# Kernel optimization log

Hardware: AMD Instinct MI355X
Metric: run time of the kernel (lower is better)

Reference implementation:

```python
import jax, jax.numpy as jnp
import numpy as np
from jax import lax

GAP_PENALTY = 0.0
TEMPERATURE = 1.0
B, A, L, D, K = 64, 26, 384, 512, 18


def setup_inputs() -> dict:
    key = jax.random.key(0)
    k1, k2, k3, k4 = jax.random.split(key, 4)
    matrices = jax.random.normal(k1, (B, A, L), dtype=jnp.float32)
    # ragged lengths: (len_i, len_0) per pair, in [L//2, L]
    shapes = jax.random.randint(k2, (B, 2), L // 2, L + 1, dtype=jnp.int32)
    s = 1.0 / np.sqrt(A * K)  # torch Conv1d default init scale
    conv_w = jax.random.uniform(k3, (D, A, K), minval=-s, maxval=s, dtype=jnp.float32)
    conv_b = jax.random.uniform(k4, (D,), minval=-s, maxval=s, dtype=jnp.float32)
    return {"matrices": matrices, "shapes": shapes, "conv_w": conv_w, "conv_b": conv_b}


def _smoothmax3(a, b, c, t):
    # t * log(exp(a/t) + exp(b/t) + exp(c/t)), numerically stable
    m = jnp.maximum(jnp.maximum(a, b), c)
    return m + t * jnp.log(jnp.exp((a - m) / t) + jnp.exp((b - m) / t) + jnp.exp((c - m) / t))


def _nw_matrix(sim, t, g):
    # sim: (L, L). Returns smoothed NW value matrix V: (L+1, L+1).
    # V[i,j] = sim[i-1,j-1] + smoothmax(V[i-1,j-1], V[i-1,j]-g, V[i,j-1]-g)
    n = sim.shape[0]
    row0 = -g * jnp.arange(n + 1, dtype=sim.dtype)  # free/affine leading gaps on top row

    def row_step(prev_row, inp):
        s_row, i = inp  # s_row: (L,)
        v_left0 = -g * i  # V[i, 0]

        def col_step(left, xs):
            s, diag, up = xs
            v = s + _smoothmax3(diag, up - g, left - g, t)
            return v, v

        _, rest = lax.scan(col_step, v_left0, (s_row, prev_row[:-1], prev_row[1:]))
        new_row = jnp.concatenate([v_left0[None], rest])
        return new_row, new_row

    _, rows = lax.scan(row_step, row0, (sim, jnp.arange(1, n + 1, dtype=sim.dtype)))
    return jnp.concatenate([row0[None], rows], axis=0)


def needleman_wunsch(sim, shapes, gap_penalty, temperature):
    # sim: (B, L, L) similarity vs sequence 0; shapes: (B, 2) int lengths.
    # Soft alignment posterior = grad of smoothed terminal score wrt similarity.
    li = jnp.clip(shapes[:, 0], 0, sim.shape[1])
    lj = jnp.clip(shapes[:, 1], 0, sim.shape[2])

    def total_score(s):
        V = jax.vmap(lambda m: _nw_matrix(m, temperature, gap_penalty))(s)  # (B, L+1, L+1)
        b = jnp.arange(s.shape[0])
        return jnp.sum(V[b, li, lj])

    return jax.grad(total_score)(sim)  # (B, L, L), expected match matrix


def reference(matrices, shapes, conv_w, conv_b):
    # Conv1d padding='same' with even kernel: torch pads (k-1)//2 left, k//2 right
    k = conv_w.shape[-1]
    pad = ((k - 1) // 2, k // 2)
    emb = lax.conv_general_dilated(
        matrices, conv_w, window_strides=(1,), padding=[pad],
        dimension_numbers=("NCH", "OIH", "NCH"),
    ) + conv_b[None, :, None]  # (B, D, L)
    e = jnp.transpose(emb, (0, 2, 1))  # (B, L, D)
    sim = jnp.einsum("bld,md->blm", e, e[0])  # (B, L_i, L_0): similarity vs sequence 0
    align = needleman_wunsch(sim, shapes, GAP_PENALTY, TEMPERATURE)  # (B, L, L)
    m = jnp.transpose(matrices, (0, 2, 1))  # (B, L, A)
    # consensus in sequence-0 coordinates, then project back to each sequence
    consensus = jnp.mean(jnp.einsum("nia,nij->nja", m, align), axis=0)  # (L, A)
    return jnp.einsum("ja,nij->nia", consensus, align)  # (B, L, A)
```

## Files before the change

kernel.cpp:

```cpp
#include <hip/hip_runtime.h>
#include <hip/hip_bf16.h>
#include <math.h>

#define B_  64
#define A_  26
#define L_  384
#define D_  512
#define K_  18
#define KC  480
#define LL  147456
#define SZD 245760

typedef __attribute__((ext_vector_type(8))) short bf16x8;
typedef __attribute__((ext_vector_type(4))) float f32x4;
typedef unsigned short ushort_t;
typedef unsigned int uint_t;

__device__ __forceinline__ void stD(float* sp, int z, int c, float v) {
    int dl = z / 6, dr = z - dl * 6;
    sp[(size_t)(dl + (c >> 2)) * 1536 + dr * 256 + dl * 4 + (c & 3)] = v;
}

__device__ __forceinline__ ushort_t f2bf(float v) {
    uint_t u = __float_as_uint(v);
    uint_t r = (u + 0x7FFFu + ((u >> 16) & 1u)) >> 16;
    return (ushort_t)r;
}

__global__ void wsplit_kernel(const float* __restrict__ w, ushort_t* __restrict__ wh,
                              ushort_t* __restrict__ wl) {
    int o = blockIdx.x * blockDim.x + threadIdx.x;
    if (o >= D_ * KC) return;
    int d = o / KC, r = o - d * KC;
    float v = (r < A_ * K_) ? w[(size_t)d * (A_ * K_) + r] : 0.0f;
    ushort_t h = f2bf(v);
    float hf = __uint_as_float(((uint_t)h) << 16);
    size_t oo = ((size_t)(r >> 5) * D_ + d) * 32 + (r & 31);
    wh[oo] = h;
    wl[oo] = f2bf(v - hf);
}

__global__ __launch_bounds__(256) void im2col_kernel(const float* __restrict__ x,
                                                     ushort_t* __restrict__ xh,
                                                     ushort_t* __restrict__ xl) {
    int b  = blockIdx.y;
    int lt = blockIdx.x;
    const float* xb = x + (size_t)b * A_ * L_;
    for (int idx = threadIdx.x; idx < 64 * KC; idx += 256) {
        int l = lt * 64 + idx / KC;
        int r = idx % KC;
        float v = 0.0f;
        if (r < A_ * K_) {
            int a = r / K_, kk = r - a * K_;
            int g = l + kk - 8;
            if (g >= 0 && g < L_) v = xb[(size_t)a * L_ + g];
        }
        ushort_t h = f2bf(v);
        float hf = __uint_as_float(((uint_t)h) << 16);
        size_t o = (((size_t)b * 15 + (r >> 5)) * L_ + l) * 32 + (r & 31);
        xh[o] = h;
        xl[o] = f2bf(v - hf);
    }
}

__global__ __launch_bounds__(256) void convmm_kernel(const ushort_t* __restrict__ xh,
                                                     const ushort_t* __restrict__ xl,
                                                     const ushort_t* __restrict__ wh,
                                                     const ushort_t* __restrict__ wl,
                                                     const float* __restrict__ bias,
                                                     ushort_t* __restrict__ ehi,
                                                     ushort_t* __restrict__ elo) {
    int b = blockIdx.z;
    int w = threadIdx.x >> 6;
    int lane = threadIdx.x & 63;
    int l0 = blockIdx.y * 64 + 32 * (w >> 1);
    int d0 = blockIdx.x * 64 + 32 * (w & 1);
    int r = lane & 15, g = lane >> 4;
    const ushort_t* pah = xh + (((size_t)b * 15) * L_ + l0 + r) * 32 + g * 8;
    const ushort_t* pal = xl + (((size_t)b * 15) * L_ + l0 + r) * 32 + g * 8;
    const ushort_t* pbh = wh + (size_t)(d0 + r) * 32 + g * 8;
    const ushort_t* pbl = wl + (size_t)(d0 + r) * 32 + g * 8;
    f32x4 acc00 = {0.f, 0.f, 0.f, 0.f}, acc01 = acc00, acc10 = acc00, acc11 = acc00;
#pragma unroll 3
    for (int ks = 0; ks < 15; ++ks) {
        size_t offA = (size_t)ks * L_ * 32;
        size_t offB = (size_t)ks * D_ * 32;
        bf16x8 Ah0 = *(const bf16x8*)(pah + offA);
        bf16x8 Ah1 = *(const bf16x8*)(pah + offA + 16 * 32);
        bf16x8 Al0 = *(const bf16x8*)(pal + offA);
        bf16x8 Al1 = *(const bf16x8*)(pal + offA + 16 * 32);
        bf16x8 Bh0 = *(const bf16x8*)(pbh + offB);
        bf16x8 Bh1 = *(const bf16x8*)(pbh + offB + 16 * 32);
        bf16x8 Bl0 = *(const bf16x8*)(pbl + offB);
        bf16x8 Bl1 = *(const bf16x8*)(pbl + offB + 16 * 32);
        acc00 = __builtin_amdgcn_mfma_f32_16x16x32_bf16(Ah0, Bh0, acc00, 0, 0, 0);
        acc00 = __builtin_amdgcn_mfma_f32_16x16x32_bf16(Ah0, Bl0, acc00, 0, 0, 0);
        acc00 = __builtin_amdgcn_mfma_f32_16x16x32_bf16(Al0, Bh0, acc00, 0, 0, 0);
        acc01 = __builtin_amdgcn_mfma_f32_16x16x32_bf16(Ah0, Bh1, acc01, 0, 0, 0);
        acc01 = __builtin_amdgcn_mfma_f32_16x16x32_bf16(Ah0, Bl1, acc01, 0, 0, 0);
        acc01 = __builtin_amdgcn_mfma_f32_16x16x32_bf16(Al0, Bh1, acc01, 0, 0, 0);
        acc10 = __builtin_amdgcn_mfma_f32_16x16x32_bf16(Ah1, Bh0, acc10, 0, 0, 0);
        acc10 = __builtin_amdgcn_mfma_f32_16x16x32_bf16(Ah1, Bl0, acc10, 0, 0, 0);
        acc10 = __builtin_amdgcn_mfma_f32_16x16x32_bf16(Al1, Bh0, acc10, 0, 0, 0);
        acc11 = __builtin_amdgcn_mfma_f32_16x16x32_bf16(Ah1, Bh1, acc11, 0, 0, 0);
        acc11 = __builtin_amdgcn_mfma_f32_16x16x32_bf16(Ah1, Bl1, acc11, 0, 0, 0);
        acc11 = __builtin_amdgcn_mfma_f32_16x16x32_bf16(Al1, Bh1, acc11, 0, 0, 0);
    }
#pragma unroll
    for (int v = 0; v < 4; ++v) {
        int lr0 = l0 + g * 4 + v, lr1 = lr0 + 16;
        int dc0 = d0 + r,         dc1 = dc0 + 16;
        float vals[4] = {acc00[v] + bias[dc0], acc01[v] + bias[dc1],
                         acc10[v] + bias[dc0], acc11[v] + bias[dc1]};
        int lrs[4] = {lr0, lr0, lr1, lr1};
        int dcs[4] = {dc0, dc1, dc0, dc1};
#pragma unroll
        for (int t = 0; t < 4; ++t) {
            ushort_t h = f2bf(vals[t]);
            float hf = __uint_as_float(((uint_t)h) << 16);
            size_t o = (((size_t)b * 16 + (dcs[t] >> 5)) * L_ + lrs[t]) * 32 + (dcs[t] & 31);
            ehi[o] = h;
            elo[o] = f2bf(vals[t] - hf);
        }
    }
}

__global__ __launch_bounds__(256) void sim_kernel(const ushort_t* __restrict__ ehi,
                                                  const ushort_t* __restrict__ elo,
                                                  float* __restrict__ simD) {
    int b = blockIdx.z;
    int w = threadIdx.x >> 6;
    int lane = threadIdx.x & 63;
    int l0 = blockIdx.y * 64 + 32 * (w >> 1);
    int m0 = blockIdx.x * 64 + 32 * (w & 1);
    int r = lane & 15, g = lane >> 4;
    const ushort_t* pah = ehi + (((size_t)b * 16) * L_ + l0 + r) * 32 + g * 8;
    const ushort_t* pal = elo + (((size_t)b * 16) * L_ + l0 + r) * 32 + g * 8;
    const ushort_t* pbh = ehi + ((size_t)(m0 + r)) * 32 + g * 8;
    const ushort_t* pbl = elo + ((size_t)(m0 + r)) * 32 + g * 8;
    f32x4 acc00 = {0.f, 0.f, 0.f, 0.f}, acc01 = acc00, acc10 = acc00, acc11 = acc00;
#pragma unroll 2
    for (int ks = 0; ks < 16; ++ks) {
        size_t off = (size_t)ks * L_ * 32;
        bf16x8 Ah0 = *(const bf16x8*)(pah + off);
        bf16x8 Ah1 = *(const bf16x8*)(pah + off + 16 * 32);
        bf16x8 Al0 = *(const bf16x8*)(pal + off);
        bf16x8 Al1 = *(const bf16x8*)(pal + off + 16 * 32);
        bf16x8 Bh0 = *(const bf16x8*)(pbh + off);
        bf16x8 Bh1 = *(const bf16x8*)(pbh + off + 16 * 32);
        bf16x8 Bl0 = *(const bf16x8*)(pbl + off);
        bf16x8 Bl1 = *(const bf16x8*)(pbl + off + 16 * 32);
        acc00 = __builtin_amdgcn_mfma_f32_16x16x32_bf16(Ah0, Bh0, acc00, 0, 0, 0);
        acc00 = __builtin_amdgcn_mfma_f32_16x16x32_bf16(Ah0, Bl0, acc00, 0, 0, 0);
        acc00 = __builtin_amdgcn_mfma_f32_16x16x32_bf16(Al0, Bh0, acc00, 0, 0, 0);
        acc01 = __builtin_amdgcn_mfma_f32_16x16x32_bf16(Ah0, Bh1, acc01, 0, 0, 0);
        acc01 = __builtin_amdgcn_mfma_f32_16x16x32_bf16(Ah0, Bl1, acc01, 0, 0, 0);
        acc01 = __builtin_amdgcn_mfma_f32_16x16x32_bf16(Al0, Bh1, acc01, 0, 0, 0);
        acc10 = __builtin_amdgcn_mfma_f32_16x16x32_bf16(Ah1, Bh0, acc10, 0, 0, 0);
        acc10 = __builtin_amdgcn_mfma_f32_16x16x32_bf16(Ah1, Bl0, acc10, 0, 0, 0);
        acc10 = __builtin_amdgcn_mfma_f32_16x16x32_bf16(Al1, Bh0, acc10, 0, 0, 0);
        acc11 = __builtin_amdgcn_mfma_f32_16x16x32_bf16(Ah1, Bh1, acc11, 0, 0, 0);
        acc11 = __builtin_amdgcn_mfma_f32_16x16x32_bf16(Ah1, Bl1, acc11, 0, 0, 0);
        acc11 = __builtin_amdgcn_mfma_f32_16x16x32_bf16(Al1, Bh1, acc11, 0, 0, 0);
    }
    float* sp = simD + (size_t)b * SZD;
#pragma unroll
    for (int v = 0; v < 4; ++v) {
        int ar0 = l0 + g * 4 + v, ar1 = ar0 + 16;
        int ac0 = m0 + r,         ac1 = ac0 + 16;
        stD(sp, ar0, ac0, acc00[v]);
        stD(sp, ar0, ac1, acc01[v]);
        stD(sp, ar1, ac0, acc10[v]);
        stD(sp, ar1, ac1, acc11[v]);
    }
}

__global__ __launch_bounds__(256, 1) void nw_fwd_kernel(const float* __restrict__ simD, float* __restrict__ VD) {
    int b = blockIdx.x;
    int tid = threadIdx.x;
    int w = tid >> 6, l = tid & 63;
    __shared__ float4 MA[4][64], MB4[4][64], MC[4][64];
    __shared__ int FL[4];
    const float4 Z4 = {0.f, 0.f, 0.f, 0.f};
    {
        int s = tid >> 6, ll = tid & 63;
        MA[s][ll] = Z4; MB4[s][ll] = Z4; MC[s][ll] = Z4;
    }
    if (tid < 4) FL[tid] = (tid == 3) ? -1 : -1000000;
    __syncthreads();
    volatile int* flg = FL;
    const float* pS = simD + (size_t)b * SZD + l * 4;
    float*       pV = VD   + (size_t)b * SZD + l * 4;
    float4 buf[6];
#pragma unroll
    for (int r = 0; r < 6; ++r) buf[r] = *(const float4*)(pS + w * 1536 + r * 256);
    int lm = (l == 0) ? 0 : (l - 1);
#pragma unroll 1
    for (int T = w; T < 159; T += 4) {
        int sp = (T - 1) & 3;
        while (flg[sp] != T - 1) {}
        asm volatile("" ::: "memory");
        float4 Ar = MA[sp][l];
        float4 Bs = MB4[sp][l];
        float4 Cs = MC[sp][l];
        float4 Bn = MB4[sp][lm];
        float4 Cn = MC[sp][lm];
        if (l == 0) { Bn = Z4; Cn = Z4; }
        float vleft[6] = {Ar.x, Ar.y, Ar.z, Ar.w, Bs.x, Bs.y};
        float d0 = Bn.z;
        float uin[4] = {Cn.x, Cn.y, Cn.z, Cn.w};
        float sc[6][4];
#pragma unroll
        for (int r = 0; r < 6; ++r) {
            sc[r][0] = buf[r].x; sc[r][1] = buf[r].y; sc[r][2] = buf[r].z; sc[r][3] = buf[r].w;
        }
        int ct = T - l;
        bool act = (ct >= 0 && ct <= 95);
        float nbc[4] = {0.f, 0.f, 0.f, 0.f}, nbp = 0.f;
        float vout[6][4];
        if (act) {
#pragma unroll
            for (int dd = 0; dd < 9; ++dd) {
#pragma unroll
                for (int r = 0; r < 6; ++r) {
                    const int q = dd - r;
                    if (q < 0 || q > 3) continue;
                    float dg = (r == 0) ? ((q == 0) ? d0 : uin[q - 1])
                                        : ((q == 0) ? vleft[r - 1] : vout[r - 1][q - 1]);
                    float up = (r == 0) ? uin[q] : vout[r - 1][q];
                    float lf = (q == 0) ? vleft[r] : vout[r][q - 1];
                    float mx = fmaxf(dg, fmaxf(up, lf));
                    vout[r][q] = sc[r][q] + mx +
                        __logf(__expf(dg - mx) + __expf(up - mx) + __expf(lf - mx));
                }
            }
            nbp = Cs.w;
#pragma unroll
            for (int q = 0; q < 4; ++q) nbc[q] = vout[5][q];
#pragma unroll
            for (int r = 0; r < 6; ++r) vleft[r] = vout[r][3];
        }
        float4 pa; pa.x = vleft[0]; pa.y = vleft[1]; pa.z = vleft[2]; pa.w = vleft[3];
        float4 pb; pb.x = vleft[4]; pb.y = vleft[5]; pb.z = nbp; pb.w = 0.f;
        float4 pc; pc.x = nbc[0]; pc.y = nbc[1]; pc.z = nbc[2]; pc.w = nbc[3];
        MA[w][l] = pa; MB4[w][l] = pb; MC[w][l] = pc;
        asm volatile("s_waitcnt lgkmcnt(0)" ::: "memory");
        if (l == 0) flg[w] = T;
        asm volatile("" ::: "memory");
        if (act) {
            float* pVd = pV + (size_t)T * 1536;
#pragma unroll
            for (int r = 0; r < 6; ++r) {
                float4 t;
                t.x = vout[r][0]; t.y = vout[r][1]; t.z = vout[r][2]; t.w = vout[r][3];
                *(float4*)(pVd + r * 256) = t;
            }
        }
        int dP = min(T + 4, 158);
#pragma unroll
        for (int r = 0; r < 6; ++r) buf[r] = *(const float4*)(pS + dP * 1536 + r * 256);
    }
}

__global__ __launch_bounds__(256, 1) void nw_bwd_kernel(const float* __restrict__ simD,
                                                        const float* __restrict__ VD,
                                                        const int* __restrict__ shapes,
                                                        float* __restrict__ ED) {
    int b = blockIdx.x;
    int tid = threadIdx.x;
    int w = tid >> 6, l = tid & 63;
    __shared__ float4 MA[4][64], MB4[4][64], MC[4][64], MD[4][64], MEx[4][64], MF[4][64];
    __shared__ int FL[4];
    const float4 Z4 = {0.f, 0.f, 0.f, 0.f};
    {
        int s = tid >> 6, ll = tid & 63;
        MA[s][ll] = Z4; MB4[s][ll] = Z4; MC[s][ll] = Z4;
        MD[s][ll] = Z4; MEx[s][ll] = Z4; MF[s][ll] = Z4;
    }
    if (tid < 4) FL[tid] = (tid == 3) ? -1 : -1000000;
    __syncthreads();
    volatile int* flg = FL;
    const float* pS = simD + (size_t)b * SZD + l * 4;
    const float* pV = VD   + (size_t)b * SZD + l * 4;
    float*       pE = ED   + (size_t)b * SZD + l * 4;
    int li = min(max(shapes[2 * b + 0], 0), L_);
    int lj = min(max(shapes[2 * b + 1], 0), L_);
    float4 bufV[6], bufS[6];
#pragma unroll
    for (int r = 0; r < 6; ++r) {
        bufV[r] = *(const float4*)(pV + (158 - w) * 1536 + r * 256);
        bufS[r] = *(const float4*)(pS + (158 - w) * 1536 + r * 256);
    }
    int lp = (l == 63) ? 63 : (l + 1);
#pragma unroll 1
    for (int T = w; T < 159; T += 4) {
        int sp = (T - 1) & 3;
        while (flg[sp] != T - 1) {}
        asm volatile("" ::: "memory");
        float4 Ar = MA[sp][l];
        float4 Br = MB4[sp][l];
        float4 Cr = MC[sp][l];
        float4 Dn = MD[sp][lp];
        float4 En = MEx[sp][lp];
        float4 Fn = MF[sp][lp];
        if (l == 63) { Dn = Z4; En = Z4; Fn = Z4; }
        float einit[6] = {Ar.x, Ar.y, Ar.z, Ar.w, Br.x, Br.y};
        float uinit[6] = {Br.z, Br.w, Cr.x, Cr.y, Cr.z, Cr.w};
        float enb_c[4] = {Dn.x, Dn.y, Dn.z, Dn.w};
        float unb_c[4] = {En.x, En.y, En.z, En.w};
        float enbtd_s = Fn.x, unbtd_s = Fn.y;
        float Vq[6][4], Sq[6][4];
#pragma unroll
        for (int r = 0; r < 6; ++r) {
            Vq[r][0] = bufV[r].x; Vq[r][1] = bufV[r].y; Vq[r][2] = bufV[r].z; Vq[r][3] = bufV[r].w;
            Sq[r][0] = bufS[r].x; Sq[r][1] = bufS[r].y; Sq[r][2] = bufS[r].z; Sq[r][3] = bufS[r].w;
        }
        int ct = 158 - T - l;
        bool act = (ct >= 0 && ct <= 95);
        float necar[4] = {0.f, 0.f, 0.f, 0.f}, nucar[4] = {0.f, 0.f, 0.f, 0.f};
        float eC[6], uC[6];
#pragma unroll
        for (int r = 0; r < 6; ++r) { eC[r] = einit[r]; uC[r] = uinit[r]; }
        float Eo[6][4];
        if (act) {
            float Uo[6][4];
#pragma unroll
            for (int r = 0; r < 6; ++r)
#pragma unroll
                for (int q = 0; q < 4; ++q)
                    Uo[r][q] = Vq[r][q] - Sq[r][q];
            float wtd[6][4], wtu[6][4], wtl[6][4];
#pragma unroll
            for (int r = 0; r < 6; ++r) {
                int i = 6 * l + r + 1;
                bool ilt = (i < L_);
#pragma unroll
                for (int q = 0; q < 4; ++q) {
                    int j = 4 * ct + q + 1;
                    bool jlt = (j < L_);
                    float ub_old = (r == 5) ? ((q == 3) ? unbtd_s : unb_c[q + 1])
                                            : ((q == 3) ? uinit[r + 1] : Uo[r + 1][q + 1]);
                    float ub_new = (r == 5) ? unb_c[q] : Uo[r + 1][q];
                    float uo_r   = (q == 3) ? uinit[r] : Uo[r][q + 1];
                    wtd[r][q] = (ilt && jlt) ? __expf(Vq[r][q] - ub_old) : 0.f;
                    wtu[r][q] = ilt ? __expf(Vq[r][q] - ub_new) : 0.f;
                    wtl[r][q] = jlt ? __expf(Vq[r][q] - uo_r) : 0.f;
                }
            }
#pragma unroll
            for (int dd = 0; dd < 9; ++dd) {
#pragma unroll
                for (int r = 5; r >= 0; --r) {
                    const int q = 8 - dd - r;
                    if (q < 0 || q > 3) continue;
                    int i = 6 * l + r + 1;
                    int j = 4 * ct + q + 1;
                    float eb_old = (r == 5) ? ((q == 3) ? enbtd_s : enb_c[q + 1])
                                            : ((q == 3) ? einit[r + 1] : Eo[r + 1][q + 1]);
                    float eb_new = (r == 5) ? enb_c[q] : Eo[r + 1][q];
                    float eo_r   = (q == 3) ? einit[r] : Eo[r][q + 1];
                    float en = (i == li && j == lj) ? 1.f : 0.f;
                    en += wtd[r][q] * eb_old + wtu[r][q] * eb_new + wtl[r][q] * eo_r;
                    Eo[r][q] = en;
                }
            }
#pragma unroll
            for (int r = 0; r < 6; ++r) { eC[r] = Eo[r][0]; uC[r] = Uo[r][0]; }
#pragma unroll
            for (int q = 0; q < 4; ++q) { necar[q] = Eo[0][q]; nucar[q] = Uo[0][q]; }
        }
        float4 pa; pa.x = eC[0]; pa.y = eC[1]; pa.z = eC[2]; pa.w = eC[3];
        float4 pb; pb.x = eC[4]; pb.y = eC[5]; pb.z = uC[0]; pb.w = uC[1];
        float4 pc; pc.x = uC[2]; pc.y = uC[3]; pc.z = uC[4]; pc.w = uC[5];
        float4 pd; pd.x = necar[0]; pd.y = necar[1]; pd.z = necar[2]; pd.w = necar[3];
        float4 pe; pe.x = nucar[0]; pe.y = nucar[1]; pe.z = nucar[2]; pe.w = nucar[3];
        float4 pf; pf.x = einit[0]; pf.y = uinit[0]; pf.z = 0.f; pf.w = 0.f;
        MA[w][l] = pa; MB4[w][l] = pb; MC[w][l] = pc;
        MD[w][l] = pd; MEx[w][l] = pe; MF[w][l] = pf;
        asm volatile("s_waitcnt lgkmcnt(0)" ::: "memory");
        if (l == 0) flg[w] = T;
        asm volatile("" ::: "memory");
        if (act) {
            float* pEd = pE + (size_t)(158 - T) * 1536;
#pragma unroll
            for (int r = 0; r < 6; ++r) {
                float4 t;
                t.x = Eo[r][0]; t.y = Eo[r][1]; t.z = Eo[r][2]; t.w = Eo[r][3];
                *(float4*)(pEd + r * 256) = t;
            }
        }
        int dP = max(158 - (T + 4), 0);
#pragma unroll
        for (int r = 0; r < 6; ++r) {
            bufV[r] = *(const float4*)(pV + dP * 1536 + r * 256);
            bufS[r] = *(const float4*)(pS + dP * 1536 + r * 256);
        }
    }
}

__global__ __launch_bounds__(256) void repack_kernel(const float* __restrict__ ED,
                                                     float* __restrict__ Enat) {
    int n  = blockIdx.y;
    int jt = blockIdx.x;
    int jl = threadIdx.x & 63;
    int gp = threadIdx.x >> 6;
    int j  = jt * 64 + jl;
    const float* eb = ED + (size_t)n * SZD + (j >> 2) * 1536 + (j & 3);
    float* ob = Enat + (size_t)n * LL + j;
#pragma unroll 4
    for (int i = gp * 96; i < gp * 96 + 96; ++i) {
        int dl = i / 6, dr = i - dl * 6;
        float v = eb[(size_t)dl * 1540 + dr * 256];
        ob[(size_t)i * L_] = v;
    }
}

__global__ __launch_bounds__(256) void consensus_kernel(const float* __restrict__ x,
                                                        const float* __restrict__ Enat,
                                                        float* __restrict__ cons) {
    int n  = blockIdx.y;
    int j0 = blockIdx.x * 64;
    __shared__ float ms[A_][L_];
    for (int idx = threadIdx.x; idx < A_ * L_; idx += 256)
        ((float*)ms)[idx] = x[(size_t)n * A_ * L_ + idx];
    __syncthreads();
    int jl = threadIdx.x & 63;
    int g  = threadIdx.x >> 6;
    int a0 = g * 7;
    int na = (a0 + 7 <= A_) ? 7 : (A_ - a0);
    int j  = j0 + jl;
    float acc[7] = {0.f, 0.f, 0.f, 0.f, 0.f, 0.f, 0.f};
    const float* aE = Enat + (size_t)n * LL + j;
    for (int i = 0; i < L_; ++i) {
        float al = aE[(size_t)i * L_];
#pragma unroll
        for (int t = 0; t < 7; ++t)
            if (t < na) acc[t] = fmaf(al, ms[a0 + t][i], acc[t]);
    }
    for (int t = 0; t < na; ++t)
        atomicAdd(&cons[(size_t)j * A_ + a0 + t], acc[t] * (1.0f / B_));
}

__global__ __launch_bounds__(256) void out_kernel(const float* __restrict__ Enat,
                                                  const float* __restrict__ cons,
                                                  float* __restrict__ out) {
    int n  = blockIdx.y;
    int i0 = blockIdx.x * 32;
    __shared__ float cs[L_][A_];
    __shared__ float as_[32][L_ + 1];
    for (int idx = threadIdx.x; idx < L_ * A_; idx += 256)
        ((float*)cs)[idx] = cons[idx];
    const float* aE = Enat + (size_t)n * LL;
    for (int idx = threadIdx.x; idx < 32 * L_; idx += 256) {
        int r = idx / L_, c = idx - r * L_;
        as_[r][c] = aE[(size_t)(i0 + r) * L_ + c];
    }
    __syncthreads();
    for (int o = threadIdx.x; o < 32 * A_; o += 256) {
        int il = o / A_, a = o % A_;
        float s = 0.f;
        for (int jj = 0; jj < L_; ++jj)
            s = fmaf(as_[il][jj], cs[jj][a], s);
        out[((size_t)n * L_ + i0 + il) * A_ + a] = s;
    }
}

extern "C" void kernel_launch(void* const* d_in, const int* in_sizes, int n_in,
                              void* d_out, int out_size, void* d_ws, size_t ws_size,
                              hipStream_t stream) {
    const float* matrices = (const float*)d_in[0];
    const int*   shapes   = (const int*)d_in[1];
    const float* conv_w   = (const float*)d_in[2];
    const float* conv_b   = (const float*)d_in[3];
    float* out = (float*)d_out;

    char* p = (char*)d_ws;
    float*    EDiag = (float*)p;
    ushort_t* xh = (ushort_t*)p;
    ushort_t* xl = xh + (size_t)B_ * 15 * L_ * 32;
    p += (size_t)B_ * SZD * 4;
    ushort_t* ehi = (ushort_t*)p;
    ushort_t* elo = ehi + (size_t)B_ * 16 * L_ * 32;
    p += (size_t)B_ * L_ * D_ * 4;
    float* simD = (float*)p;
    float* Enat = simD;
    p += (size_t)B_ * SZD * 4;
    float* VD = (float*)p;
    p += (size_t)B_ * SZD * 4;
    ushort_t* wh = (ushort_t*)p;
    ushort_t* wl = wh + (size_t)15 * D_ * 32;
    p += (size_t)15 * D_ * 32 * 4;
    float* cons = (float*)p;

    wsplit_kernel<<<(D_ * KC + 255) / 256, 256, 0, stream>>>(conv_w, wh, wl);
    im2col_kernel<<<dim3(L_ / 64, B_), 256, 0, stream>>>(matrices, xh, xl);
    convmm_kernel<<<dim3(D_ / 64, L_ / 64, B_), 256, 0, stream>>>(xh, xl, wh, wl, conv_b, ehi, elo);
    sim_kernel<<<dim3(L_ / 64, L_ / 64, B_), 256, 0, stream>>>(ehi, elo, simD);
    nw_fwd_kernel<<<B_, 256, 0, stream>>>(simD, VD);
    nw_bwd_kernel<<<B_, 256, 0, stream>>>(simD, VD, shapes, EDiag);
    repack_kernel<<<dim3(L_ / 64, B_), 256, 0, stream>>>(EDiag, Enat);
    hipMemsetAsync(cons, 0, (size_t)L_ * A_ * sizeof(float), stream);
    consensus_kernel<<<dim3(L_ / 64, B_), 256, 0, stream>>>(matrices, Enat, cons);
    out_kernel<<<dim3(L_ / 32, B_), 256, 0, stream>>>(Enat, cons, out);
}
```

Before: 930.9 us.

## Precompute backward NW weights before spin-wait; simplify forward logsumexp with med3

The backward wavefront kernel now loads the neighbouring U values (V minus sim) directly from global memory instead of receiving them through shared memory from the previous wave. That moves all exp weight computation and delta masks ahead of the spin-wait on the dependency flag, which shortens the serial critical path and trims the shared-memory handoff. The forward kernel uses min/med3/max so the logsumexp needs two exps instead of three. In exchange there are extra scalar global loads per step and more live registers. A leftover duplicate assignment suggests the code was rushed, and loads at the edges may read neighbouring padded data.

```diff
diff --git a/kernel.cpp b/kernel.cpp
--- a/kernel.cpp
+++ b/kernel.cpp
@@ -230,8 +230,10 @@
                     float up = (r == 0) ? uin[q] : vout[r - 1][q];
                     float lf = (q == 0) ? vleft[r] : vout[r][q - 1];
                     float mx = fmaxf(dg, fmaxf(up, lf));
+                    float mn = fminf(dg, fminf(up, lf));
+                    float md = __builtin_amdgcn_fmed3f(dg, up, lf);
                     vout[r][q] = sc[r][q] + mx +
-                        __logf(__expf(dg - mx) + __expf(up - mx) + __expf(lf - mx));
+                        __logf(1.0f + (__expf(md - mx) + __expf(mn - mx)));
                 }
             }
             nbp = Cs.w;
@@ -269,114 +271,125 @@
     int b = blockIdx.x;
     int tid = threadIdx.x;
     int w = tid >> 6, l = tid & 63;
-    __shared__ float4 MA[4][64], MB4[4][64], MC[4][64], MD[4][64], MEx[4][64], MF[4][64];
+    __shared__ float4 MA[4][64], MB4[4][64], MD[4][64], MF[4][64];
     __shared__ int FL[4];
     const float4 Z4 = {0.f, 0.f, 0.f, 0.f};
     {
         int s = tid >> 6, ll = tid & 63;
-        MA[s][ll] = Z4; MB4[s][ll] = Z4; MC[s][ll] = Z4;
-        MD[s][ll] = Z4; MEx[s][ll] = Z4; MF[s][ll] = Z4;
+        MA[s][ll] = Z4; MB4[s][ll] = Z4; MD[s][ll] = Z4; MF[s][ll] = Z4;
     }
     if (tid < 4) FL[tid] = (tid == 3) ? -1 : -1000000;
     __syncthreads();
     volatile int* flg = FL;
-    const float* pS = simD + (size_t)b * SZD + l * 4;
-    const float* pV = VD   + (size_t)b * SZD + l * 4;
-    float*       pE = ED   + (size_t)b * SZD + l * 4;
+    const float* pS  = simD + (size_t)b * SZD + l * 4;
+    const float* pV  = VD   + (size_t)b * SZD + l * 4;
+    const float* pSn = simD + (size_t)b * SZD + (l + 1) * 4;
+    const float* pVn = VD   + (size_t)b * SZD + (l + 1) * 4;
+    float*       pE  = ED   + (size_t)b * SZD + l * 4;
     int li = min(max(shapes[2 * b + 0], 0), L_);
     int lj = min(max(shapes[2 * b + 1], 0), L_);
-    float4 bufV[6], bufS[6];
-#pragma unroll
-    for (int r = 0; r < 6; ++r) {
-        bufV[r] = *(const float4*)(pV + (158 - w) * 1536 + r * 256);
-        bufS[r] = *(const float4*)(pS + (158 - w) * 1536 + r * 256);
+    float4 bufV[6], bufS[6], bufV2, bufS2;
+    float bufV1x[6], bufS1x[6], bufV2bx, bufS2bx;
+    {
+        int dp = 158 - w;
+#pragma unroll
+        for (int r = 0; r < 6; ++r) {
+            bufV[r] = *(const float4*)(pV + dp * 1536 + r * 256);
+            bufS[r] = *(const float4*)(pS + dp * 1536 + r * 256);
+            bufV1x[r] = *(pV + (dp + 1) * 1536 + r * 256);
+            bufS1x[r] = *(pS + (dp + 1) * 1536 + r * 256);
+        }
+        bufV2 = *(const float4*)(pVn + (dp + 1) * 1536);
+        bufS2 = *(const float4*)(pSn + (dp + 1) * 1536);
+        bufV2bx = *(pVn + (dp + 2) * 1536 - 1536);
+        bufV2bx = *(pVn + min(dp + 2, 159) * 1536);
+        bufS2bx = *(pSn + min(dp + 2, 159) * 1536);
     }
     int lp = (l == 63) ? 63 : (l + 1);
 #pragma unroll 1
     for (int T = w; T < 159; T += 4) {
+        int ct = 158 - T - l;
+        bool act = (ct >= 0 && ct <= 95);
+        float Vq[6][4], Sq[6][4];
+#pragma unroll
+        for (int r = 0; r < 6; ++r) {
+            Vq[r][0] = bufV[r].x; Vq[r][1] = bufV[r].y; Vq[r][2] = bufV[r].z; Vq[r][3] = bufV[r].w;
+            Sq[r][0] = bufS[r].x; Sq[r][1] = bufS[r].y; Sq[r][2] = bufS[r].z; Sq[r][3] = bufS[r].w;
+        }
+        float uin1[6];
+#pragma unroll
+        for (int r = 0; r < 6; ++r) uin1[r] = bufV1x[r] - bufS1x[r];
+        float U2[4] = {bufV2.x - bufS2.x, bufV2.y - bufS2.y,
+                       bufV2.z - bufS2.z, bufV2.w - bufS2.w};
+        float u2s = bufV2bx - bufS2bx;
+        float Uo[6][4];
+#pragma unroll
+        for (int r = 0; r < 6; ++r)
+#pragma unroll
+            for (int q = 0; q < 4; ++q)
+                Uo[r][q] = Vq[r][q] - Sq[r][q];
+        float wtd[6][4], wtu[6][4], wtl[6][4], del[6][4];
+#pragma unroll
+        for (int r = 0; r < 6; ++r) {
+            int i = 6 * l + r + 1;
+            bool ilt = (i < L_);
+#pragma unroll
+            for (int q = 0; q < 4; ++q) {
+                int j = 4 * ct + q + 1;
+                bool jlt = (j < L_);
+                float ub_old = (r == 5) ? ((q == 3) ? u2s : U2[q + 1])
+                                        : ((q == 3) ? uin1[r + 1] : Uo[r + 1][q + 1]);
+                float ub_new = (r == 5) ? U2[q] : Uo[r + 1][q];
+                float uo_r   = (q == 3) ? uin1[r] : Uo[r][q + 1];
+                wtd[r][q] = (ilt && jlt) ? __expf(Vq[r][q] - ub_old) : 0.f;
+                wtu[r][q] = ilt ? __expf(Vq[r][q] - ub_new) : 0.f;
+                wtl[r][q] = jlt ? __expf(Vq[r][q] - uo_r) : 0.f;
+                del[r][q] = (i == li && j == lj) ? 1.f : 0.f;
+            }
+        }
+        __builtin_amdgcn_sched_barrier(0);
         int sp = (T - 1) & 3;
         while (flg[sp] != T - 1) {}
         asm volatile("" ::: "memory");
         float4 Ar = MA[sp][l];
         float4 Br = MB4[sp][l];
-        float4 Cr = MC[sp][l];
         float4 Dn = MD[sp][lp];
-        float4 En = MEx[sp][lp];
         float4 Fn = MF[sp][lp];
-        if (l == 63) { Dn = Z4; En = Z4; Fn = Z4; }
+        if (l == 63) { Dn = Z4; Fn = Z4; }
         float einit[6] = {Ar.x, Ar.y, Ar.z, Ar.w, Br.x, Br.y};
-        float uinit[6] = {Br.z, Br.w, Cr.x, Cr.y, Cr.z, Cr.w};
         float enb_c[4] = {Dn.x, Dn.y, Dn.z, Dn.w};
-        float unb_c[4] = {En.x, En.y, En.z, En.w};
-        float enbtd_s = Fn.x, unbtd_s = Fn.y;
-        float Vq[6][4], Sq[6][4];
-#pragma unroll
-        for (int r = 0; r < 6; ++r) {
-            Vq[r][0] = bufV[r].x; Vq[r][1] = bufV[r].y; Vq[r][2] = bufV[r].z; Vq[r][3] = bufV[r].w;
-            Sq[r][0] = bufS[r].x; Sq[r][1] = bufS[r].y; Sq[r][2] = bufS[r].z; Sq[r][3] = bufS[r].w;
-        }
-        int ct = 158 - T - l;
-        bool act = (ct >= 0 && ct <= 95);
-        float necar[4] = {0.f, 0.f, 0.f, 0.f}, nucar[4] = {0.f, 0.f, 0.f, 0.f};
-        float eC[6], uC[6];
-#pragma unroll
-        for (int r = 0; r < 6; ++r) { eC[r] = einit[r]; uC[r] = uinit[r]; }
+        float enbtd_s = Fn.x;
+        float necar[4] = {0.f, 0.f, 0.f, 0.f};
+        float eC[6];
+#pragma unroll
+        for (int r = 0; r < 6; ++r) eC[r] = einit[r];
         float Eo[6][4];
         if (act) {
-            float Uo[6][4];
-#pragma unroll
-            for (int r = 0; r < 6; ++r)
-#pragma unroll
-                for (int q = 0; q < 4; ++q)
-                    Uo[r][q] = Vq[r][q] - Sq[r][q];
-            float wtd[6][4], wtu[6][4], wtl[6][4];
-#pragma unroll
-            for (int r = 0; r < 6; ++r) {
-                int i = 6 * l + r + 1;
-                bool ilt = (i < L_);
-#pragma unroll
-                for (int q = 0; q < 4; ++q) {
-                    int j = 4 * ct + q + 1;
-                    bool jlt = (j < L_);
-                    float ub_old = (r == 5) ? ((q == 3) ? unbtd_s : unb_c[q + 1])
-                                            : ((q == 3) ? uinit[r + 1] : Uo[r + 1][q + 1]);
-                    float ub_new = (r == 5) ? unb_c[q] : Uo[r + 1][q];
-                    float uo_r   = (q == 3) ? uinit[r] : Uo[r][q + 1];
-                    wtd[r][q] = (ilt && jlt) ? __expf(Vq[r][q] - ub_old) : 0.f;
-                    wtu[r][q] = ilt ? __expf(Vq[r][q] - ub_new) : 0.f;
-                    wtl[r][q] = jlt ? __expf(Vq[r][q] - uo_r) : 0.f;
-                }
-            }
 #pragma unroll
             for (int dd = 0; dd < 9; ++dd) {
 #pragma unroll
                 for (int r = 5; r >= 0; --r) {
                     const int q = 8 - dd - r;
                     if (q < 0 || q > 3) continue;
-                    int i = 6 * l + r + 1;
-                    int j = 4 * ct + q + 1;
                     float eb_old = (r == 5) ? ((q == 3) ? enbtd_s : enb_c[q + 1])
                                             : ((q == 3) ? einit[r + 1] : Eo[r + 1][q + 1]);
                     float eb_new = (r == 5) ? enb_c[q] : Eo[r + 1][q];
                     float eo_r   = (q == 3) ? einit[r] : Eo[r][q + 1];
-                    float en = (i == li && j == lj) ? 1.f : 0.f;
+                    float en = del[r][q];
                     en += wtd[r][q] * eb_old + wtu[r][q] * eb_new + wtl[r][q] * eo_r;
                     Eo[r][q] = en;
                 }
             }
 #pragma unroll
-            for (int r = 0; r < 6; ++r) { eC[r] = Eo[r][0]; uC[r] = Uo[r][0]; }
-#pragma unroll
-            for (int q = 0; q < 4; ++q) { necar[q] = Eo[0][q]; nucar[q] = Uo[0][q]; }
+            for (int r = 0; r < 6; ++r) eC[r] = Eo[r][0];
+#pragma unroll
+            for (int q = 0; q < 4; ++q) necar[q] = Eo[0][q];
         }
         float4 pa; pa.x = eC[0]; pa.y = eC[1]; pa.z = eC[2]; pa.w = eC[3];
-        float4 pb; pb.x = eC[4]; pb.y = eC[5]; pb.z = uC[0]; pb.w = uC[1];
-        float4 pc; pc.x = uC[2]; pc.y = uC[3]; pc.z = uC[4]; pc.w = uC[5];
+        float4 pb; pb.x = eC[4]; pb.y = eC[5]; pb.z = 0.f; pb.w = 0.f;
         float4 pd; pd.x = necar[0]; pd.y = necar[1]; pd.z = necar[2]; pd.w = necar[3];
-        float4 pe; pe.x = nucar[0]; pe.y = nucar[1]; pe.z = nucar[2]; pe.w = nucar[3];
-        float4 pf; pf.x = einit[0]; pf.y = uinit[0]; pf.z = 0.f; pf.w = 0.f;
-        MA[w][l] = pa; MB4[w][l] = pb; MC[w][l] = pc;
-        MD[w][l] = pd; MEx[w][l] = pe; MF[w][l] = pf;
+        float4 pf; pf.x = einit[0]; pf.y = 0.f; pf.z = 0.f; pf.w = 0.f;
+        MA[w][l] = pa; MB4[w][l] = pb; MD[w][l] = pd; MF[w][l] = pf;
         asm volatile("s_waitcnt lgkmcnt(0)" ::: "memory");
         if (l == 0) flg[w] = T;
         asm volatile("" ::: "memory");
@@ -389,12 +402,18 @@
                 *(float4*)(pEd + r * 256) = t;
             }
         }
-        int dP = max(158 - (T + 4), 0);
+        int dp = max(158 - (T + 4), 0);
 #pragma unroll
         for (int r = 0; r < 6; ++r) {
-            bufV[r] = *(const float4*)(pV + dP * 1536 + r * 256);
-            bufS[r] = *(const float4*)(pS + dP * 1536 + r * 256);
-        }
+            bufV[r] = *(const float4*)(pV + dp * 1536 + r * 256);
+            bufS[r] = *(const float4*)(pS + dp * 1536 + r * 256);
+            bufV1x[r] = *(pV + (dp + 1) * 1536 + r * 256);
+            bufS1x[r] = *(pS + (dp + 1) * 1536 + r * 256);
+        }
+        bufV2 = *(const float4*)(pVn + (dp + 1) * 1536);
+        bufS2 = *(const float4*)(pSn + (dp + 1) * 1536);
+        bufV2bx = *(pVn + min(dp + 2, 159) * 1536);
+        bufS2bx = *(pSn + min(dp + 2, 159) * 1536);
     }
 }
 
```

After: 900.8 us. 1.03x faster.
